# Kernel optimization log

Hardware: AMD Instinct MI355X
Metric: run time of the kernel (lower is better)

## Reference

```python
import jax, jax.numpy as jnp
import numpy as np

N_NODES = 100000
N_EDGES = 6400000
D_FEAT = 128
HIDDEN = 16


def _gcn_conv(x, row, col, W, b, n):
    # PyG GCNConv: add self-loops, symmetric norm, message from row -> aggregated at col
    h = x @ W  # [N, out]
    loop = jnp.arange(n, dtype=row.dtype)
    r = jnp.concatenate([row, loop])
    c = jnp.concatenate([col, loop])
    ones = jnp.ones(r.shape[0], dtype=x.dtype)
    deg = jax.ops.segment_sum(ones, c, num_segments=n)  # in-degree incl. self-loop
    dinv = jnp.where(deg > 0, jax.lax.rsqrt(deg), 0.0)
    norm = dinv[r] * dinv[c]  # [E+N]
    msg = h[r] * norm[:, None]  # [E+N, out]
    out = jax.ops.segment_sum(msg, c, num_segments=n)
    return out + b


def setup_inputs() -> dict:
    key = jax.random.key(0)
    ks = jax.random.split(key, 8)
    x = jax.random.normal(ks[0], (N_NODES, D_FEAT), dtype=jnp.float32)
    edge_attr = jax.random.normal(ks[1], (N_EDGES, 1), dtype=jnp.float32)
    edge_row = jnp.sort(jax.random.randint(ks[2], (N_EDGES,), 0, N_NODES, dtype=jnp.int32)).astype(jnp.int64)
    edge_col = jax.random.randint(ks[3], (N_EDGES,), 0, N_NODES, dtype=jnp.int32).astype(jnp.int64)
    W1 = jax.random.normal(ks[4], (D_FEAT + 1, HIDDEN), dtype=jnp.float32) * (1.0 / np.sqrt(D_FEAT + 1))
    b1 = jnp.zeros((HIDDEN,), dtype=jnp.float32)
    W2 = jax.random.normal(ks[5], (HIDDEN, 1), dtype=jnp.float32) * (1.0 / np.sqrt(HIDDEN))
    b2 = jnp.zeros((1,), dtype=jnp.float32)
    return {"x": x, "edge_attr": edge_attr, "edge_row": edge_row, "edge_col": edge_col,
            "W1": W1, "b1": b1, "W2": W2, "b2": b2}


def reference(x, edge_attr, edge_row, edge_col, W1, b1, W2, b2):
    n = x.shape[0]
    # the original Python loop == segment-sum of edge_attr by source node (rows are sorted)
    x_edge = jax.ops.segment_sum(edge_attr, edge_row, num_segments=n)  # [N, 1]
    h = jnp.concatenate([x, x_edge], axis=1)  # [N, D+1]
    h = _gcn_conv(h, edge_row, edge_col, W1, b1, n)
    h = jax.nn.relu(h)
    # dropout is identity in eval mode
    out = _gcn_conv(h, edge_row, edge_col, W2, b2, n)  # [N, 1]
    return out
```

## Files before the change

### kernel.cpp

```cpp
#include <hip/hip_runtime.h>


#define D_FEAT 128
#define HIDDEN 16
#define TILE 4096
#define CAP 17408u

__device__ inline float bf2f(unsigned short u) {
    union { unsigned x; float f; } t; t.x = ((unsigned)u) << 16; return t.f;
}

__global__ __launch_bounds__(256) void k_init(float* xe, unsigned* gcur, int n, int nb) {
    int t = blockIdx.x * 256 + threadIdx.x;
    if (t < n) xe[t] = 0.f;
    if (t < nb) gcur[t * 16] = (unsigned)t * CAP;
}

__global__ __launch_bounds__(512) void k_sortplace(const int* __restrict__ row,
                                                   const int* __restrict__ col,
                                                   const float* __restrict__ ea,
                                                   float* __restrict__ xe,
                                                   unsigned* __restrict__ gcur,
                                                   unsigned* __restrict__ ebufP,
                                                   int ne, int nb) {
    __shared__ unsigned stage[TILE];
    __shared__ unsigned short sbuck[TILE];
    __shared__ unsigned h[512], base_[512], cursor[512], gb_[512];
    __shared__ unsigned wsum[8];
    int tid = threadIdx.x;
    int lane = tid & 63;
    int w = tid >> 6;
    int tile0 = blockIdx.x * TILE;
    int cnt_t = min(TILE, ne - tile0);
    h[tid] = 0u;
    __syncthreads();
    int rr[8], cc[8];
    float aa[8];
    #pragma unroll
    for (int k = 0; k < 8; ++k) {
        int e = tile0 + tid + k * 512;
        if (e < ne) {
            rr[k] = row[e]; cc[k] = col[e]; aa[k] = ea[e];
            atomicAdd(&h[cc[k] >> 8], 1u);
        } else { rr[k] = -1; cc[k] = 0; aa[k] = 0.f; }
    }
    #pragma unroll
    for (int k = 0; k < 8; ++k) {
        int r = rr[k];
        float a = aa[k];
        #pragma unroll
        for (int d = 1; d < 64; d <<= 1) {
            float up = __shfl_up(a, d);
            int  rup = __shfl_up(r, d);
            if (lane >= d && rup == r) a += up;
        }
        int rdn = __shfl_down(r, 1);
        bool tail = (lane == 63) || (rdn != r);
        if (r >= 0 && tail) unsafeAtomicAdd(&xe[r], a);
    }
    __syncthreads();
    unsigned hv = h[tid];
    unsigned s = hv;
    #pragma unroll
    for (int d = 1; d < 64; d <<= 1) {
        unsigned u = __shfl_up(s, d);
        if (lane >= d) s += u;
    }
    if (lane == 63) wsum[w] = s;
    __syncthreads();
    unsigned woff = 0;
    #pragma unroll
    for (int i = 0; i < 8; ++i) woff += (i < w) ? wsum[i] : 0u;
    unsigned ex = s + woff - hv;
    base_[tid] = ex;
    cursor[tid] = ex;
    if (tid < nb && hv) gb_[tid] = atomicAdd(&gcur[tid * 16], hv);
    __syncthreads();
    #pragma unroll
    for (int k = 0; k < 8; ++k) {
        if (rr[k] >= 0) {
            int b = cc[k] >> 8;
            unsigned p = atomicAdd(&cursor[b], 1u);
            stage[p] = (((unsigned)(cc[k] & 255)) << 24) | (unsigned)rr[k];
            sbuck[p] = (unsigned short)b;
        }
    }
    __syncthreads();
    for (int t = tid; t < cnt_t; t += 512) {
        unsigned b = sbuck[t];
        unsigned pos = gb_[b] + ((unsigned)t - base_[b]);
        if (pos < (b + 1u) * CAP) ebufP[pos] = stage[t];
    }
}

__global__ __launch_bounds__(512) void k_deghist(const unsigned* __restrict__ gcur,
                                                 const unsigned* __restrict__ ebufP,
                                                 unsigned* __restrict__ deg, int n) {
    __shared__ unsigned dg[256];
    int tid = threadIdx.x, b = blockIdx.x;
    if (tid < 256) dg[tid] = 0u;
    __syncthreads();
    unsigned base = (unsigned)b * CAP;
    unsigned m = min(gcur[b * 16] - base, CAP);
    unsigned i = tid;
    for (; i + 1536 < m; i += 2048) {
        unsigned pk0 = ebufP[base + i];
        unsigned pk1 = ebufP[base + i + 512];
        unsigned pk2 = ebufP[base + i + 1024];
        unsigned pk3 = ebufP[base + i + 1536];
        atomicAdd(&dg[pk0 >> 24], 1u);
        atomicAdd(&dg[pk1 >> 24], 1u);
        atomicAdd(&dg[pk2 >> 24], 1u);
        atomicAdd(&dg[pk3 >> 24], 1u);
    }
    for (; i < m; i += 512) atomicAdd(&dg[ebufP[base + i] >> 24], 1u);
    __syncthreads();
    if (tid < 256) {
        int v = b * 256 + tid;
        if (v < n) deg[v] = dg[tid];
    }
}

__global__ __launch_bounds__(256) void k_gemm1(const float* __restrict__ x,
                                               const float* __restrict__ xe,
                                               const unsigned* __restrict__ deg,
                                               const float* __restrict__ W1,
                                               float* __restrict__ g,
                                               unsigned short* __restrict__ gb, int n) {
    __shared__ float WsT[16 * 132];
    __shared__ float xs[64 * 132];
    int tid = threadIdx.x;
    for (int idx = tid; idx < 129 * 16; idx += 256) {
        int k = idx >> 4, j = idx & 15;
        WsT[j * 132 + k] = W1[idx];
    }
    int n0 = blockIdx.x * 64;
    const float4* x4 = (const float4*)x;
    for (int idx = tid; idx < 64 * 32; idx += 256) {
        int r = idx >> 5, c = idx & 31;
        float4 v = (n0 + r < n) ? x4[(size_t)(n0 + r) * 32 + c]
                                : make_float4(0.f, 0.f, 0.f, 0.f);
        *(float4*)&xs[r * 132 + c * 4] = v;
    }
    if (tid < 64) {
        int r = tid;
        xs[r * 132 + 128] = (n0 + r < n) ? xe[n0 + r] : 0.f;
    }
    __syncthreads();
    int j  = tid & 15;
    int nb = tid >> 4;
    const float* wrow = &WsT[j * 132];
    for (int rep = 0; rep < 4; ++rep) {
        int nl = nb + (rep << 4);
        int node = n0 + nl;
        const float* xrow = &xs[nl * 132];
        float acc = 0.f;
        #pragma unroll
        for (int k = 0; k < 128; k += 4) {
            float4 xv = *(const float4*)&xrow[k];
            float4 wv = *(const float4*)&wrow[k];
            acc += xv.x * wv.x;
            acc += xv.y * wv.y;
            acc += xv.z * wv.z;
            acc += xv.w * wv.w;
        }
        acc += xrow[128] * wrow[128];
        if (node < n) {
            float v = acc * rsqrtf((float)deg[node] + 1.0f);
            g[(size_t)node * 16 + j] = v;
            union { float f; unsigned u; } cv; cv.f = v;
            unsigned r16 = (cv.u + 0x7FFFu + ((cv.u >> 16) & 1u)) >> 16;
            gb[(size_t)node * 16 + j] = (unsigned short)r16;
        }
    }
}

__global__ __launch_bounds__(512) void k_agg1s(const unsigned* __restrict__ gcur,
                                               const unsigned* __restrict__ ebufP,
                                               const unsigned* __restrict__ deg,
                                               const unsigned* __restrict__ gu,
                                               const float* __restrict__ g,
                                               const float* __restrict__ b1,
                                               const float* __restrict__ W2,
                                               float* __restrict__ g2, int n) {
    __shared__ unsigned sorted[CAP];
    __shared__ unsigned dg[256], st[256], cur[256];
    __shared__ unsigned wsum[4];
    int tid = threadIdx.x, b = blockIdx.x, lane = tid & 63;
    unsigned base = (unsigned)b * CAP;
    unsigned m = min(gcur[b * 16] - base, CAP);
    unsigned dval = 0, s = 0;
    if (tid < 256) {
        int v = b * 256 + tid;
        dval = (v < n) ? deg[v] : 0u;
        dg[tid] = dval;
        s = dval;
        #pragma unroll
        for (int d = 1; d < 64; d <<= 1) {
            unsigned uu = __shfl_up(s, d);
            if (lane >= d) s += uu;
        }
        if (lane == 63) wsum[tid >> 6] = s;
    }
    __syncthreads();
    if (tid < 256) {
        int w = tid >> 6;
        unsigned woff = 0;
        #pragma unroll
        for (int i = 0; i < 4; ++i) woff += (i < w) ? wsum[i] : 0u;
        unsigned ex = s + woff - dval;
        st[tid] = ex;
        cur[tid] = ex;
    }
    __syncthreads();
    unsigned i = tid;
    for (; i + 1536 < m; i += 2048) {
        unsigned pk0 = ebufP[base + i];
        unsigned pk1 = ebufP[base + i + 512];
        unsigned pk2 = ebufP[base + i + 1024];
        unsigned pk3 = ebufP[base + i + 1536];
        unsigned p0 = atomicAdd(&cur[pk0 >> 24], 1u);
        unsigned p1 = atomicAdd(&cur[pk1 >> 24], 1u);
        unsigned p2 = atomicAdd(&cur[pk2 >> 24], 1u);
        unsigned p3 = atomicAdd(&cur[pk3 >> 24], 1u);
        if (p0 < CAP) sorted[p0] = pk0 & 0xFFFFFFu;
        if (p1 < CAP) sorted[p1] = pk1 & 0xFFFFFFu;
        if (p2 < CAP) sorted[p2] = pk2 & 0xFFFFFFu;
        if (p3 < CAP) sorted[p3] = pk3 & 0xFFFFFFu;
    }
    for (; i < m; i += 512) {
        unsigned pk = ebufP[base + i];
        unsigned p = atomicAdd(&cur[pk >> 24], 1u);
        if (p < CAP) sorted[p] = pk & 0xFFFFFFu;
    }
    __syncthreads();
    const uint2* gu2 = (const uint2*)gu;
    int grp = tid >> 4;
    int u = tid & 3;
    int quarter = (tid >> 2) & 3;
    float4 bb = ((const float4*)b1)[u];
    float4 ww = ((const float4*)W2)[u];
    for (int it = 0; it < 8; ++it) {
        int c = it * 32 + grp;
        int v = b * 256 + c;
        if (v >= n) break;
        unsigned s0 = st[c], e0 = s0 + dg[c];
        float a0 = 0.f, a1 = 0.f, a2 = 0.f, a3 = 0.f;
        float c0 = 0.f, c1 = 0.f, c2 = 0.f, c3 = 0.f;
        unsigned q = s0 + quarter;
        for (; q + 4 < e0; q += 8) {
            unsigned r0 = sorted[q], r1 = sorted[q + 4];
            uint2 w0 = gu2[(size_t)r0 * 4 + u];
            uint2 w1 = gu2[(size_t)r1 * 4 + u];
            a0 += bf2f((unsigned short)w0.x); a1 += bf2f((unsigned short)(w0.x >> 16));
            a2 += bf2f((unsigned short)w0.y); a3 += bf2f((unsigned short)(w0.y >> 16));
            c0 += bf2f((unsigned short)w1.x); c1 += bf2f((unsigned short)(w1.x >> 16));
            c2 += bf2f((unsigned short)w1.y); c3 += bf2f((unsigned short)(w1.y >> 16));
        }
        for (; q < e0; q += 4) {
            uint2 w0 = gu2[(size_t)sorted[q] * 4 + u];
            a0 += bf2f((unsigned short)w0.x); a1 += bf2f((unsigned short)(w0.x >> 16));
            a2 += bf2f((unsigned short)w0.y); a3 += bf2f((unsigned short)(w0.y >> 16));
        }
        a0 += c0; a1 += c1; a2 += c2; a3 += c3;
        a0 += __shfl_xor(a0, 4, 16); a0 += __shfl_xor(a0, 8, 16);
        a1 += __shfl_xor(a1, 4, 16); a1 += __shfl_xor(a1, 8, 16);
        a2 += __shfl_xor(a2, 4, 16); a2 += __shfl_xor(a2, 8, 16);
        a3 += __shfl_xor(a3, 4, 16); a3 += __shfl_xor(a3, 8, 16);
        float di = rsqrtf((float)dg[c] + 1.0f);
        float4 gs = ((const float4*)g)[(size_t)v * 4 + u];
        float v0 = fmaxf(di * (gs.x + a0) + bb.x, 0.f);
        float v1 = fmaxf(di * (gs.y + a1) + bb.y, 0.f);
        float v2 = fmaxf(di * (gs.z + a2) + bb.z, 0.f);
        float v3 = fmaxf(di * (gs.w + a3) + bb.w, 0.f);
        float prd = v0 * ww.x + v1 * ww.y + v2 * ww.z + v3 * ww.w;
        prd += __shfl_down(prd, 2, 4);
        prd += __shfl_down(prd, 1, 4);
        if ((tid & 15) == 0) g2[v] = prd * di;
    }
}

__global__ __launch_bounds__(512) void k_agg2s(const unsigned* __restrict__ gcur,
                                               const unsigned* __restrict__ ebufP,
                                               const unsigned* __restrict__ deg,
                                               const float* __restrict__ g2,
                                               const float* __restrict__ b2,
                                               float* __restrict__ out, int n) {
    __shared__ unsigned sorted[CAP];
    __shared__ unsigned dg[256], st[256], cur[256];
    __shared__ unsigned wsum[4];
    int tid = threadIdx.x, b = blockIdx.x, lane = tid & 63;
    unsigned base = (unsigned)b * CAP;
    unsigned m = min(gcur[b * 16] - base, CAP);
    unsigned dval = 0, s = 0;
    if (tid < 256) {
        int v = b * 256 + tid;
        dval = (v < n) ? deg[v] : 0u;
        dg[tid] = dval;
        s = dval;
        #pragma unroll
        for (int d = 1; d < 64; d <<= 1) {
            unsigned uu = __shfl_up(s, d);
            if (lane >= d) s += uu;
        }
        if (lane == 63) wsum[tid >> 6] = s;
    }
    __syncthreads();
    if (tid < 256) {
        int w = tid >> 6;
        unsigned woff = 0;
        #pragma unroll
        for (int i = 0; i < 4; ++i) woff += (i < w) ? wsum[i] : 0u;
        unsigned ex = s + woff - dval;
        st[tid] = ex;
        cur[tid] = ex;
    }
    __syncthreads();
    unsigned i = tid;
    for (; i + 1536 < m; i += 2048) {
        unsigned pk0 = ebufP[base + i];
        unsigned pk1 = ebufP[base + i + 512];
        unsigned pk2 = ebufP[base + i + 1024];
        unsigned pk3 = ebufP[base + i + 1536];
        unsigned p0 = atomicAdd(&cur[pk0 >> 24], 1u);
        unsigned p1 = atomicAdd(&cur[pk1 >> 24], 1u);
        unsigned p2 = atomicAdd(&cur[pk2 >> 24], 1u);
        unsigned p3 = atomicAdd(&cur[pk3 >> 24], 1u);
        if (p0 < CAP) sorted[p0] = pk0 & 0xFFFFFFu;
        if (p1 < CAP) sorted[p1] = pk1 & 0xFFFFFFu;
        if (p2 < CAP) sorted[p2] = pk2 & 0xFFFFFFu;
        if (p3 < CAP) sorted[p3] = pk3 & 0xFFFFFFu;
    }
    for (; i < m; i += 512) {
        unsigned pk = ebufP[base + i];
        unsigned p = atomicAdd(&cur[pk >> 24], 1u);
        if (p < CAP) sorted[p] = pk & 0xFFFFFFu;
    }
    __syncthreads();
    int c = tid >> 1, half = tid & 1;
    int v = b * 256 + c;
    float a = 0.f;
    unsigned s0 = st[c], e0 = s0 + dg[c];
    unsigned q = s0 + half;
    for (; q + 2 < e0; q += 4) {
        a += g2[sorted[q]];
        a += g2[sorted[q + 2]];
    }
    if (q < e0) a += g2[sorted[q]];
    a += __shfl_xor(a, 1, 2);
    if (half == 0 && v < n) {
        float di = rsqrtf((float)dg[c] + 1.0f);
        out[v] = di * (g2[v] + a) + b2[0];
    }
}

extern "C" void kernel_launch(void* const* d_in, const int* in_sizes, int n_in,
                              void* d_out, int out_size, void* d_ws, size_t ws_size,
                              hipStream_t stream) {
    const float* x   = (const float*)d_in[0];
    const float* ea  = (const float*)d_in[1];
    const int*   row = (const int*)d_in[2];
    const int*   col = (const int*)d_in[3];
    const float* W1  = (const float*)d_in[4];
    const float* b1  = (const float*)d_in[5];
    const float* W2  = (const float*)d_in[6];
    const float* b2  = (const float*)d_in[7];
    float* out = (float*)d_out;

    int n  = in_sizes[0] / D_FEAT;
    int ne = in_sizes[2];
    int nb = (n + 255) >> 8;

    float* ws   = (float*)d_ws;
    float* xe   = ws;
    float* g    = ws + (size_t)n;
    float* g2   = ws + (size_t)17 * n;
    unsigned short* gbuf = (unsigned short*)(ws + (size_t)18 * n);
    unsigned* deg  = (unsigned*)(ws + (size_t)26 * n);
    unsigned* gcur = deg + (size_t)n;
    unsigned* ebufP = gcur + (size_t)nb * 16;

    dim3 blk(256);
    int g_node = (n + 255) / 256;
    int g_tile = (ne + TILE - 1) / TILE;
    int g_gemm = (n + 63) / 64;

    k_init<<<g_node, blk, 0, stream>>>(xe, gcur, n, nb);
    k_sortplace<<<g_tile, 512, 0, stream>>>(row, col, ea, xe, gcur, ebufP, ne, nb);
    k_deghist<<<nb, 512, 0, stream>>>(gcur, ebufP, deg, n);
    k_gemm1<<<g_gemm, blk, 0, stream>>>(x, xe, deg, W1, g, gbuf, n);
    k_agg1s<<<nb, 512, 0, stream>>>(gcur, ebufP, deg, (const unsigned*)gbuf, g, b1, W2, g2, n);
    k_agg2s<<<nb, 512, 0, stream>>>(gcur, ebufP, deg, g2, b2, out, n);
}
```

Baseline: 293.6 us.

## Persist per-bucket sorted edge lists and reuse them in second-layer aggregation

The per-bucket exclusive scan of degrees moves into the degree-histogram kernel and is stored as global start offsets. The first aggregation kernel writes its LDS-sorted source lists to a global buffer. The second aggregation kernel then becomes a light gather kernel over that buffer, dropping the repeated bucket counting sort and its large LDS allocation. The cost is an extra global write and read of the sorted edge lists, plus more workspace.

```diff
diff --git a/kernel.cpp b/kernel.cpp
--- a/kernel.cpp
+++ b/kernel.cpp
@@ -95,9 +95,11 @@
 
 __global__ __launch_bounds__(512) void k_deghist(const unsigned* __restrict__ gcur,
                                                  const unsigned* __restrict__ ebufP,
-                                                 unsigned* __restrict__ deg, int n) {
+                                                 unsigned* __restrict__ deg,
+                                                 unsigned* __restrict__ stG, int n) {
     __shared__ unsigned dg[256];
-    int tid = threadIdx.x, b = blockIdx.x;
+    __shared__ unsigned wsum[4];
+    int tid = threadIdx.x, b = blockIdx.x, lane = tid & 63;
     if (tid < 256) dg[tid] = 0u;
     __syncthreads();
     unsigned base = (unsigned)b * CAP;
@@ -115,9 +117,26 @@
     }
     for (; i < m; i += 512) atomicAdd(&dg[ebufP[base + i] >> 24], 1u);
     __syncthreads();
+    unsigned dval = 0, s = 0;
     if (tid < 256) {
+        dval = dg[tid];
+        s = dval;
+        #pragma unroll
+        for (int d = 1; d < 64; d <<= 1) {
+            unsigned uu = __shfl_up(s, d);
+            if (lane >= d) s += uu;
+        }
+        if (lane == 63) wsum[tid >> 6] = s;
+    }
+    __syncthreads();
+    if (tid < 256) {
+        int w = tid >> 6;
+        unsigned woff = 0;
+        #pragma unroll
+        for (int i2 = 0; i2 < 4; ++i2) woff += (i2 < w) ? wsum[i2] : 0u;
+        unsigned ex = s + woff - dval;
         int v = b * 256 + tid;
-        if (v < n) deg[v] = dg[tid];
+        if (v < n) { deg[v] = dval; stG[v] = base + ex; }
     }
 }
 
@@ -178,39 +197,25 @@
 __global__ __launch_bounds__(512) void k_agg1s(const unsigned* __restrict__ gcur,
                                                const unsigned* __restrict__ ebufP,
                                                const unsigned* __restrict__ deg,
+                                               const unsigned* __restrict__ stG,
                                                const unsigned* __restrict__ gu,
                                                const float* __restrict__ g,
                                                const float* __restrict__ b1,
                                                const float* __restrict__ W2,
-                                               float* __restrict__ g2, int n) {
+                                               float* __restrict__ g2,
+                                               unsigned* __restrict__ sortedG, int n) {
     __shared__ unsigned sorted[CAP];
     __shared__ unsigned dg[256], st[256], cur[256];
-    __shared__ unsigned wsum[4];
-    int tid = threadIdx.x, b = blockIdx.x, lane = tid & 63;
+    int tid = threadIdx.x, b = blockIdx.x;
     unsigned base = (unsigned)b * CAP;
     unsigned m = min(gcur[b * 16] - base, CAP);
-    unsigned dval = 0, s = 0;
     if (tid < 256) {
         int v = b * 256 + tid;
-        dval = (v < n) ? deg[v] : 0u;
+        unsigned dval = (v < n) ? deg[v] : 0u;
+        unsigned sv   = (v < n) ? stG[v] - base : 0u;
         dg[tid] = dval;
-        s = dval;
-        #pragma unroll
-        for (int d = 1; d < 64; d <<= 1) {
-            unsigned uu = __shfl_up(s, d);
-            if (lane >= d) s += uu;
-        }
-        if (lane == 63) wsum[tid >> 6] = s;
-    }
-    __syncthreads();
-    if (tid < 256) {
-        int w = tid >> 6;
-        unsigned woff = 0;
-        #pragma unroll
-        for (int i = 0; i < 4; ++i) woff += (i < w) ? wsum[i] : 0u;
-        unsigned ex = s + woff - dval;
-        st[tid] = ex;
-        cur[tid] = ex;
+        st[tid] = sv;
+        cur[tid] = sv;
     }
     __syncthreads();
     unsigned i = tid;
@@ -234,6 +239,7 @@
         if (p < CAP) sorted[p] = pk & 0xFFFFFFu;
     }
     __syncthreads();
+    for (unsigned t = tid; t < m; t += 512) sortedG[base + t] = sorted[t];
     const uint2* gu2 = (const uint2*)gu;
     int grp = tid >> 4;
     int u = tid & 3;
@@ -280,76 +286,31 @@
     }
 }
 
-__global__ __launch_bounds__(512) void k_agg2s(const unsigned* __restrict__ gcur,
-                                               const unsigned* __restrict__ ebufP,
+__global__ __launch_bounds__(256) void k_agg2w(const unsigned* __restrict__ stG,
                                                const unsigned* __restrict__ deg,
+                                               const unsigned* __restrict__ sortedG,
                                                const float* __restrict__ g2,
                                                const float* __restrict__ b2,
                                                float* __restrict__ out, int n) {
-    __shared__ unsigned sorted[CAP];
-    __shared__ unsigned dg[256], st[256], cur[256];
-    __shared__ unsigned wsum[4];
-    int tid = threadIdx.x, b = blockIdx.x, lane = tid & 63;
-    unsigned base = (unsigned)b * CAP;
-    unsigned m = min(gcur[b * 16] - base, CAP);
-    unsigned dval = 0, s = 0;
-    if (tid < 256) {
-        int v = b * 256 + tid;
-        dval = (v < n) ? deg[v] : 0u;
-        dg[tid] = dval;
-        s = dval;
-        #pragma unroll
-        for (int d = 1; d < 64; d <<= 1) {
-            unsigned uu = __shfl_up(s, d);
-            if (lane >= d) s += uu;
-        }
-        if (lane == 63) wsum[tid >> 6] = s;
-    }
-    __syncthreads();
-    if (tid < 256) {
-        int w = tid >> 6;
-        unsigned woff = 0;
-        #pragma unroll
-        for (int i = 0; i < 4; ++i) woff += (i < w) ? wsum[i] : 0u;
-        unsigned ex = s + woff - dval;
-        st[tid] = ex;
-        cur[tid] = ex;
-    }
-    __syncthreads();
-    unsigned i = tid;
-    for (; i + 1536 < m; i += 2048) {
-        unsigned pk0 = ebufP[base + i];
-        unsigned pk1 = ebufP[base + i + 512];
-        unsigned pk2 = ebufP[base + i + 1024];
-        unsigned pk3 = ebufP[base + i + 1536];
-        unsigned p0 = atomicAdd(&cur[pk0 >> 24], 1u);
-        unsigned p1 = atomicAdd(&cur[pk1 >> 24], 1u);
-        unsigned p2 = atomicAdd(&cur[pk2 >> 24], 1u);
-        unsigned p3 = atomicAdd(&cur[pk3 >> 24], 1u);
-        if (p0 < CAP) sorted[p0] = pk0 & 0xFFFFFFu;
-        if (p1 < CAP) sorted[p1] = pk1 & 0xFFFFFFu;
-        if (p2 < CAP) sorted[p2] = pk2 & 0xFFFFFFu;
-        if (p3 < CAP) sorted[p3] = pk3 & 0xFFFFFFu;
-    }
-    for (; i < m; i += 512) {
-        unsigned pk = ebufP[base + i];
-        unsigned p = atomicAdd(&cur[pk >> 24], 1u);
-        if (p < CAP) sorted[p] = pk & 0xFFFFFFu;
-    }
-    __syncthreads();
-    int c = tid >> 1, half = tid & 1;
-    int v = b * 256 + c;
-    float a = 0.f;
-    unsigned s0 = st[c], e0 = s0 + dg[c];
-    unsigned q = s0 + half;
-    for (; q + 2 < e0; q += 4) {
-        a += g2[sorted[q]];
-        a += g2[sorted[q + 2]];
-    }
-    if (q < e0) a += g2[sorted[q]];
-    a += __shfl_xor(a, 1, 2);
-    if (half == 0 && v < n) {
-        float di = rsqrtf((float)dg[c] + 1.0f);
+    int tid = threadIdx.x;
+    int c = tid >> 2, u = tid & 3;
+    int v = blockIdx.x * 64 + c;
+    if (v >= n) return;
+    unsigned s0 = stG[v];
+    unsigned d  = deg[v];
+    unsigned e0 = s0 + d;
+    float a0 = 0.f, a1 = 0.f;
+    unsigned q = s0 + u;
+    for (; q + 4 < e0; q += 8) {
+        a0 += g2[sortedG[q]];
+        a1 += g2[sortedG[q + 4]];
+    }
+    for (; q < e0; q += 4) a0 += g2[sortedG[q]];
+    float a = a0 + a1;
+    a += __shfl_down(a, 2, 4);
+    a += __shfl_down(a, 1, 4);
+    if (u == 0) {
+        float di = rsqrtf((float)d + 1.0f);
         out[v] = di * (g2[v] + a) + b2[0];
     }
 }
@@ -377,18 +338,21 @@
     float* g2   = ws + (size_t)17 * n;
     unsigned short* gbuf = (unsigned short*)(ws + (size_t)18 * n);
     unsigned* deg  = (unsigned*)(ws + (size_t)26 * n);
-    unsigned* gcur = deg + (size_t)n;
-    unsigned* ebufP = gcur + (size_t)nb * 16;
+    unsigned* stG  = deg + (size_t)n;
+    unsigned* gcur = stG + (size_t)n;
+    unsigned* ebufP   = gcur + (size_t)nb * 16;
+    unsigned* sortedG = ebufP + (size_t)nb * CAP;
 
     dim3 blk(256);
     int g_node = (n + 255) / 256;
     int g_tile = (ne + TILE - 1) / TILE;
     int g_gemm = (n + 63) / 64;
+    int g_n64  = (n + 63) / 64;
 
     k_init<<<g_node, blk, 0, stream>>>(xe, gcur, n, nb);
     k_sortplace<<<g_tile, 512, 0, stream>>>(row, col, ea, xe, gcur, ebufP, ne, nb);
-    k_deghist<<<nb, 512, 0, stream>>>(gcur, ebufP, deg, n);
+    k_deghist<<<nb, 512, 0, stream>>>(gcur, ebufP, deg, stG, n);
     k_gemm1<<<g_gemm, blk, 0, stream>>>(x, xe, deg, W1, g, gbuf, n);
-    k_agg1s<<<nb, 512, 0, stream>>>(gcur, ebufP, deg, (const unsigned*)gbuf, g, b1, W2, g2, n);
-    k_agg2s<<<nb, 512, 0, stream>>>(gcur, ebufP, deg, g2, b2, out, n);
-}
+    k_agg1s<<<nb, 512, 0, stream>>>(gcur, ebufP, deg, stG, (const unsigned*)gbuf, g, b1, W2, g2, sortedG, n);
+    k_agg2w<<<g_n64, blk, 0, stream>>>(stG, deg, sortedG, g2, b2, out, n);
+}
```

Measured after the change: 303.5 us. +3.3%, slower.
